# Optimization experiments

Measured on AMD Instinct MI355X. Metric: run time of the kernel, lower is better.

The kernel has to match this reference:

```python
import jax, jax.numpy as jnp
import numpy as np

NUM_EMBEDDINGS = 512
EMBEDDING_DIM = 64
COMMITMENT_COST = 0.25


def setup_inputs() -> dict:
    key = jax.random.key(0)
    k1, k2 = jax.random.split(key)
    x = jax.random.normal(k1, (32, 64, 64, 64), dtype=jnp.float32)  # [B, C=D, H, W]
    # torch init: uniform(-1/K, 1/K)
    w = jax.random.uniform(k2, (NUM_EMBEDDINGS, EMBEDDING_DIM), dtype=jnp.float32,
                           minval=-1.0 / NUM_EMBEDDINGS, maxval=1.0 / NUM_EMBEDDINGS)
    return {"x": x, "w": w}


def reference(x, w):
    # [B, C, H, W] -> [B, H, W, C]
    xt = jnp.transpose(x, (0, 2, 3, 1))
    flat = xt.reshape(-1, EMBEDDING_DIM)  # [N, D]
    # squared L2 distances to each codebook vector: [N, K]
    distances = (jnp.sum(flat * flat, axis=1, keepdims=True)
                 + jnp.sum(w * w, axis=1)
                 - 2.0 * flat @ w.T)
    idx = jnp.argmin(distances, axis=1)  # [N]
    encodings = jax.nn.one_hot(idx, NUM_EMBEDDINGS, dtype=x.dtype)  # [N, K]
    quantized = w[idx].reshape(xt.shape)  # gather == one_hot @ w
    e_latent_loss = jnp.mean((jax.lax.stop_gradient(quantized) - xt) ** 2)
    q_latent_loss = jnp.mean((quantized - jax.lax.stop_gradient(xt)) ** 2)
    quant_loss = q_latent_loss + COMMITMENT_COST * e_latent_loss
    # straight-through estimator
    quantized_st = xt + jax.lax.stop_gradient(quantized - xt)
    quantized_out = jnp.transpose(quantized_st, (0, 3, 1, 2))  # back to [B, C, H, W]
    avg_probs = jnp.mean(encodings, axis=0)
    perplexity = jnp.exp(-jnp.sum(avg_probs * jnp.log(avg_probs + 1e-10)))
    return quantized_out, quant_loss, encodings, perplexity
```

## Files before the change

### kernel.cpp

```cpp
#include <hip/hip_runtime.h>
#include <math.h>

#define TB        256
#define POSB      64
#define NPOS      131072
#define KCODES    512
#define DIM       64
#define HW        4096
#define LOSS_OFF  8388608ull
#define ENC_OFF   8388609ull
#define PERP_OFF  75497473ull
#define TILE_DW   (POSB * KCODES)
#define NF4       ((TILE_DW - 4) / 4)
#define TAU       2.0e-4f

typedef __attribute__((ext_vector_type(8))) short bf16x8;
typedef __attribute__((ext_vector_type(4))) float f32x4;

__device__ __forceinline__ float tree8(float r0, float r1, float r2, float r3,
                                       float r4, float r5, float r6, float r7) {
    return __fadd_rn(__fadd_rn(__fadd_rn(r0, r1), __fadd_rn(r2, r3)),
                     __fadd_rn(__fadd_rn(r4, r5), __fadd_rn(r6, r7)));
}

extern "C" __global__ __launch_bounds__(512)
void vq_prep(const float* __restrict__ w, float* __restrict__ ww,
             int* __restrict__ counts, float* __restrict__ lossAcc,
             unsigned short* __restrict__ wfrag)
{
    const int k = threadIdx.x;
    const float* wk = w + k * DIM;
    const int ct = k >> 4, n = k & 15;
    float r[8];
    #pragma unroll
    for (int i = 0; i < 8; ++i) {
        #pragma unroll
        for (int j = 0; j < 8; ++j) {
            const int d = i * 8 + j;
            float v = wk[d];
            float pp = __fmul_rn(v, v);
            r[j] = (i == 0) ? pp : __fadd_rn(r[j], pp);
            unsigned int hb = __float_as_uint(v) & 0xFFFF0000u;
            float rr = v - __uint_as_float(hb);
            unsigned short hs = (unsigned short)(hb >> 16);
            unsigned short ls = (unsigned short)(__float_as_uint(rr) >> 16);
            const int q = d >> 5, kk = d & 31;
            const int lf = ((kk >> 3) << 4) + n, j8 = kk & 7;
            wfrag[((((0 * 32 + ct) * 2 + q) * 64 + lf) << 3) + j8] = hs;
            wfrag[((((1 * 32 + ct) * 2 + q) * 64 + lf) << 3) + j8] = ls;
        }
    }
    ww[k] = tree8(r[0], r[1], r[2], r[3], r[4], r[5], r[6], r[7]);
    counts[k] = 0;
    if (k == 0) *lossAcc = 0.0f;
}

#define FRAG(PART, CT, Q) wf[((((PART) * 32 + (CT)) * 2 + (Q)) * 64) + l]

#define TILE6(BH0, BH1, BL0, BL1, WWK)                                        \
    acc = (f32x4){(WWK), (WWK), (WWK), (WWK)};                                \
    acc = __builtin_amdgcn_mfma_f32_16x16x32_bf16(aL0, BH0, acc, 0, 0, 0);    \
    acc = __builtin_amdgcn_mfma_f32_16x16x32_bf16(aH0, BL0, acc, 0, 0, 0);    \
    acc = __builtin_amdgcn_mfma_f32_16x16x32_bf16(aH0, BH0, acc, 0, 0, 0);    \
    acc = __builtin_amdgcn_mfma_f32_16x16x32_bf16(aL1, BH1, acc, 0, 0, 0);    \
    acc = __builtin_amdgcn_mfma_f32_16x16x32_bf16(aH1, BL1, acc, 0, 0, 0);    \
    acc = __builtin_amdgcn_mfma_f32_16x16x32_bf16(aH1, BH1, acc, 0, 0, 0);

extern "C" __global__ __launch_bounds__(TB)
__attribute__((amdgpu_waves_per_eu(3, 8)))
void vq_main(const float* __restrict__ x, const float* __restrict__ w,
             const float* __restrict__ ww, float* __restrict__ out,
             int* __restrict__ counts, float* __restrict__ lossAcc,
             const unsigned short* __restrict__ wfrag)
{
    __shared__ __align__(16) float xtile[DIM][65];
    __shared__ float wwlds[KCODES];
    __shared__ int   hcount[KCODES];
    __shared__ int   ccount[POSB];
    __shared__ int   clist[POSB * 4];
    __shared__ int   bestkL[POSB];

    const int tid = threadIdx.x;
    const int l   = tid & 63;
    const int wv  = tid >> 6;
    const int n0  = blockIdx.x * POSB;
    const int b   = n0 >> 12;
    const int hw0 = n0 & 4095;

    hcount[tid]      = 0;
    hcount[tid + TB] = 0;
    if (tid < POSB) ccount[tid] = 0;
    wwlds[tid]      = ww[tid];
    wwlds[tid + TB] = ww[tid + TB];

    const float* xb = x + ((size_t)b * DIM) * HW + hw0;
    #pragma unroll
    for (int it = 0; it < 16; ++it) {
        const int idx = it * TB + tid;
        const int d = idx >> 6, ps = idx & 63;
        xtile[d][ps] = xb[(size_t)d * HW + ps];
    }

    const size_t T0 = ENC_OFF + (size_t)blockIdx.x * TILE_DW;
    float4* zs4 = reinterpret_cast<float4*>(out + T0 + 3);
    const float4 zero4 = make_float4(0.0f, 0.0f, 0.0f, 0.0f);
    if (tid < 3)  out[T0 + tid] = 0.0f;
    if (tid == 3) out[T0 + (TILE_DW - 1)] = 0.0f;

    __syncthreads();

    bf16x8 aH0, aH1, aL0, aL1;
    {
        const int arow = wv * 16 + (l & 15);
        #pragma unroll
        for (int q = 0; q < 2; ++q) {
            #pragma unroll
            for (int j8 = 0; j8 < 8; ++j8) {
                const int d = q * 32 + ((l >> 4) << 3) + j8;
                float v = xtile[d][arow];
                float m2 = -(v + v);
                unsigned int hb = __float_as_uint(m2) & 0xFFFF0000u;
                float rr = m2 - __uint_as_float(hb);
                short hs = (short)(hb >> 16);
                short ls = (short)(__float_as_uint(rr) >> 16);
                if (q == 0) { aH0[j8] = hs; aL0[j8] = ls; }
                else        { aH1[j8] = hs; aL1[j8] = ls; }
            }
        }
    }

    const bf16x8* wf = reinterpret_cast<const bf16x8*>(wfrag);
    const int rb = wv * 16 + ((l >> 4) << 2);

    float rmin[4] = { INFINITY, INFINITY, INFINITY, INFINITY };
    {
        bf16x8 c0 = FRAG(0, 0, 0), c1 = FRAG(0, 0, 1);
        bf16x8 c2 = FRAG(1, 0, 0), c3 = FRAG(1, 0, 1);
        float wa = wwlds[(l & 15)];
        f32x4 acc;
        #pragma unroll 1
        for (int ct = 0; ct < 32; ct += 2) {
            bf16x8 n0_ = FRAG(0, ct + 1, 0), n1_ = FRAG(0, ct + 1, 1);
            bf16x8 n2_ = FRAG(1, ct + 1, 0), n3_ = FRAG(1, ct + 1, 1);
            float wb = wwlds[(ct + 1) * 16 + (l & 15)];
            TILE6(c0, c1, c2, c3, wa)
            #pragma unroll
            for (int i = 0; i < 4; ++i) rmin[i] = fminf(rmin[i], acc[i]);
            {   const int m = (ct >> 1) * TB + tid;
                if (m < NF4) zs4[m] = zero4; }
            const int t2 = (ct + 2) & 31;
            c0 = FRAG(0, t2, 0); c1 = FRAG(0, t2, 1);
            c2 = FRAG(1, t2, 0); c3 = FRAG(1, t2, 1);
            wa = wwlds[t2 * 16 + (l & 15)];
            TILE6(n0_, n1_, n2_, n3_, wb)
            #pragma unroll
            for (int i = 0; i < 4; ++i) rmin[i] = fminf(rmin[i], acc[i]);
        }
    }
    #pragma unroll
    for (int mm = 1; mm < 16; mm <<= 1) {
        #pragma unroll
        for (int i = 0; i < 4; ++i)
            rmin[i] = fminf(rmin[i], __shfl_xor(rmin[i], mm));
    }
    float thr[4];
    #pragma unroll
    for (int i = 0; i < 4; ++i) thr[i] = rmin[i] + TAU;

    {
        bf16x8 c0 = FRAG(0, 0, 0), c1 = FRAG(0, 0, 1);
        bf16x8 c2 = FRAG(1, 0, 0), c3 = FRAG(1, 0, 1);
        float wa = wwlds[(l & 15)];
        f32x4 acc;
        #pragma unroll 1
        for (int ct = 0; ct < 32; ct += 2) {
            bf16x8 n0_ = FRAG(0, ct + 1, 0), n1_ = FRAG(0, ct + 1, 1);
            bf16x8 n2_ = FRAG(1, ct + 1, 0), n3_ = FRAG(1, ct + 1, 1);
            float wb = wwlds[(ct + 1) * 16 + (l & 15)];
            TILE6(c0, c1, c2, c3, wa)
            #pragma unroll
            for (int i = 0; i < 4; ++i) {
                if (acc[i] <= thr[i]) {
                    int s = atomicAdd(&ccount[rb + i], 1);
                    if (s < 4) clist[(rb + i) * 4 + s] = ct * 16 + (l & 15);
                }
            }
            {   const int m = (16 + (ct >> 1)) * TB + tid;
                if (m < NF4) zs4[m] = zero4; }
            const int t2 = (ct + 2) & 31;
            c0 = FRAG(0, t2, 0); c1 = FRAG(0, t2, 1);
            c2 = FRAG(1, t2, 0); c3 = FRAG(1, t2, 1);
            wa = wwlds[t2 * 16 + (l & 15)];
            TILE6(n0_, n1_, n2_, n3_, wb)
            #pragma unroll
            for (int i = 0; i < 4; ++i) {
                if (acc[i] <= thr[i]) {
                    int s = atomicAdd(&ccount[rb + i], 1);
                    if (s < 4) clist[(rb + i) * 4 + s] = (ct + 1) * 16 + (l & 15);
                }
            }
        }
    }

    __syncthreads();

    if (wv == 0) {
        const int cnt = ccount[l];
        int bk;
        if (cnt == 1) {
            bk = clist[l * 4 + 0];
        } else {
            float x2c[DIM];
            float r[8];
            #pragma unroll
            for (int d = 0; d < DIM; ++d) {
                float v = xtile[d][l];
                x2c[d] = v + v;
                float pp = __fmul_rn(v, v);
                r[d & 7] = (d < 8) ? pp : __fadd_rn(r[d & 7], pp);
            }
            const float A = tree8(r[0], r[1], r[2], r[3], r[4], r[5], r[6], r[7]);
            if (cnt <= 4) {
                float bd = INFINITY; int bk2 = KCODES;
                for (int c = 0; c < cnt; ++c) {
                    const int k = clist[l * 4 + c];
                    const float* wk = w + (size_t)k * DIM;
                    float s[8];
                    #pragma unroll
                    for (int i = 0; i < 8; ++i) {
                        #pragma unroll
                        for (int j = 0; j < 8; ++j) {
                            const int d = i * 8 + j;
                            float wvv = wk[d];
                            if (i == 0) s[j] = __fmul_rn(x2c[d], wvv);
                            else        s[j] = __fmaf_rn(x2c[d], wvv, s[j]);
                        }
                    }
                    float dot  = tree8(s[0], s[1], s[2], s[3], s[4], s[5], s[6], s[7]);
                    float dist = __fadd_rn(__fadd_rn(A, wwlds[k]), -dot);
                    if (dist < bd || (dist == bd && k < bk2)) { bd = dist; bk2 = k; }
                }
                bk = bk2;
            } else {
                float bd = INFINITY; int bk2 = 0;
                #pragma unroll 1
                for (int k = 0; k < KCODES; ++k) {
                    const float* wk = w + (size_t)k * DIM;
                    float s[8];
                    #pragma unroll
                    for (int i = 0; i < 8; ++i) {
                        #pragma unroll
                        for (int j = 0; j < 8; ++j) {
                            const int d = i * 8 + j;
                            float wvv = wk[d];
                            if (i == 0) s[j] = __fmul_rn(x2c[d], wvv);
                            else        s[j] = __fmaf_rn(x2c[d], wvv, s[j]);
                        }
                    }
                    float dot  = tree8(s[0], s[1], s[2], s[3], s[4], s[5], s[6], s[7]);
                    float dist = __fadd_rn(__fadd_rn(A, wwlds[k]), -dot);
                    if (dist < bd) { bd = dist; bk2 = k; }
                }
                bk = bk2;
            }
        }
        bestkL[l] = bk;
        out[ENC_OFF + (size_t)(n0 + l) * KCODES + bk] = 1.0f;
        atomicAdd(&hcount[bk], 1);
    }

    __syncthreads();

    {
        const int sp = tid & 63, q = tid >> 6;
        const int bk = bestkL[sp];
        const float4* wr = reinterpret_cast<const float4*>(w + (size_t)bk * DIM);
        float* qo = out + ((size_t)b * DIM) * HW + (hw0 + sp);
        float sse = 0.0f;
        #pragma unroll
        for (int c = 0; c < 4; ++c) {
            float4 qv = wr[q * 4 + c];
            const int ch = q * 16 + c * 4;
            qo[(size_t)(ch + 0) * HW] = qv.x;
            qo[(size_t)(ch + 1) * HW] = qv.y;
            qo[(size_t)(ch + 2) * HW] = qv.z;
            qo[(size_t)(ch + 3) * HW] = qv.w;
            float e0 = qv.x - xtile[ch + 0][sp]; sse = __fmaf_rn(e0, e0, sse);
            float e1 = qv.y - xtile[ch + 1][sp]; sse = __fmaf_rn(e1, e1, sse);
            float e2 = qv.z - xtile[ch + 2][sp]; sse = __fmaf_rn(e2, e2, sse);
            float e3 = qv.w - xtile[ch + 3][sp]; sse = __fmaf_rn(e3, e3, sse);
        }
        #pragma unroll
        for (int off = 32; off > 0; off >>= 1) sse += __shfl_down(sse, off);
        if (l == 0) atomicAdd(lossAcc, sse);
    }

    __syncthreads();

    {
        int c0 = hcount[tid];       if (c0) atomicAdd(&counts[tid], c0);
        int c1 = hcount[tid + TB];  if (c1) atomicAdd(&counts[tid + TB], c1);
    }
}

extern "C" __global__ __launch_bounds__(512)
void vq_finalize(const int* __restrict__ counts, const float* __restrict__ lossAcc,
                 float* __restrict__ out)
{
    __shared__ double sred[KCODES];
    const int t = threadIdx.x;
    double p = (double)counts[t] * (1.0 / (double)NPOS);
    sred[t] = -p * log(p + 1e-10);
    __syncthreads();
    for (int s = KCODES / 2; s > 0; s >>= 1) {
        if (t < s) sred[t] += sred[t + s];
        __syncthreads();
    }
    if (t == 0) {
        out[PERP_OFF] = (float)exp(sred[0]);
        out[LOSS_OFF] = 1.25f * (lossAcc[0] / 8388608.0f);
    }
}

extern "C" void kernel_launch(void* const* d_in, const int* in_sizes, int n_in,
                              void* d_out, int out_size, void* d_ws, size_t ws_size,
                              hipStream_t stream)
{
    const float* x = (const float*)d_in[0];
    const float* w = (const float*)d_in[1];
    float* out = (float*)d_out;

    float* ww              = (float*)d_ws;
    int*   counts          = (int*)((char*)d_ws + 2048);
    float* lossAcc         = (float*)((char*)d_ws + 4096);
    unsigned short* wfrag  = (unsigned short*)((char*)d_ws + 8192);

    vq_prep<<<1, 512, 0, stream>>>(w, ww, counts, lossAcc, wfrag);
    vq_main<<<NPOS / POSB, TB, 0, stream>>>(x, w, ww, out, counts,
                                            lossAcc, wfrag);
    vq_finalize<<<1, 512, 0, stream>>>(counts, lossAcc, out);
}
```

Before: 439.2 us.

## Move one-hot encoding writes out of main kernel into separate streaming kernel

The main VQ kernel no longer zero-fills the 256MB one-hot encoding tile inside its MFMA loops and no longer scatters the 1.0 value. It writes each position's best code index to a small workspace buffer instead. A new kernel then writes the full encodings, each float4 computed directly from that index. This decouples the compute-bound distance search from the bandwidth-bound store, at the cost of an extra launch and a small index round-trip through global memory.

```diff
diff --git a/kernel.cpp b/kernel.cpp
--- a/kernel.cpp
+++ b/kernel.cpp
@@ -71,7 +71,8 @@
 void vq_main(const float* __restrict__ x, const float* __restrict__ w,
              const float* __restrict__ ww, float* __restrict__ out,
              int* __restrict__ counts, float* __restrict__ lossAcc,
-             const unsigned short* __restrict__ wfrag)
+             const unsigned short* __restrict__ wfrag,
+             unsigned short* __restrict__ bkg)
 {
     __shared__ __align__(16) float xtile[DIM][65];
     __shared__ float wwlds[KCODES];
@@ -100,13 +101,6 @@
         const int d = idx >> 6, ps = idx & 63;
         xtile[d][ps] = xb[(size_t)d * HW + ps];
     }
-
-    const size_t T0 = ENC_OFF + (size_t)blockIdx.x * TILE_DW;
-    float4* zs4 = reinterpret_cast<float4*>(out + T0 + 3);
-    const float4 zero4 = make_float4(0.0f, 0.0f, 0.0f, 0.0f);
-    if (tid < 3)  out[T0 + tid] = 0.0f;
-    if (tid == 3) out[T0 + (TILE_DW - 1)] = 0.0f;
-
     __syncthreads();
 
     bf16x8 aH0, aH1, aL0, aL1;
@@ -146,8 +140,6 @@
             TILE6(c0, c1, c2, c3, wa)
             #pragma unroll
             for (int i = 0; i < 4; ++i) rmin[i] = fminf(rmin[i], acc[i]);
-            {   const int m = (ct >> 1) * TB + tid;
-                if (m < NF4) zs4[m] = zero4; }
             const int t2 = (ct + 2) & 31;
             c0 = FRAG(0, t2, 0); c1 = FRAG(0, t2, 1);
             c2 = FRAG(1, t2, 0); c3 = FRAG(1, t2, 1);
@@ -185,8 +177,6 @@
                     if (s < 4) clist[(rb + i) * 4 + s] = ct * 16 + (l & 15);
                 }
             }
-            {   const int m = (16 + (ct >> 1)) * TB + tid;
-                if (m < NF4) zs4[m] = zero4; }
             const int t2 = (ct + 2) & 31;
             c0 = FRAG(0, t2, 0); c1 = FRAG(0, t2, 1);
             c2 = FRAG(1, t2, 0); c3 = FRAG(1, t2, 1);
@@ -265,7 +255,7 @@
             }
         }
         bestkL[l] = bk;
-        out[ENC_OFF + (size_t)(n0 + l) * KCODES + bk] = 1.0f;
+        bkg[n0 + l] = (unsigned short)bk;
         atomicAdd(&hcount[bk], 1);
     }
 
@@ -303,6 +293,41 @@
     }
 }
 
+extern "C" __global__ __launch_bounds__(TB)
+void vq_enc(const unsigned short* __restrict__ bkg, float* __restrict__ out)
+{
+    __shared__ int bkL[POSB];
+    const int tid = threadIdx.x;
+    const int n0  = blockIdx.x * POSB;
+    if (tid < POSB) bkL[tid] = bkg[n0 + tid];
+    const size_t T0 = ENC_OFF + (size_t)blockIdx.x * TILE_DW;
+    __syncthreads();
+
+    if (tid < 3)  out[T0 + tid] = (bkL[0] == tid) ? 1.0f : 0.0f;
+    if (tid == 3) out[T0 + (TILE_DW - 1)] = (bkL[POSB - 1] == 511) ? 1.0f : 0.0f;
+
+    float4* zs4 = reinterpret_cast<float4*>(out + T0 + 3);
+    #pragma unroll 4
+    for (int it = 0; it < 32; ++it) {
+        const int m = it * TB + tid;
+        if (m < NF4) {
+            const int o0 = 3 + 4 * m;
+            float4 v;
+            {
+                const int oa = o0,     pa = oa >> 9, ca = oa & 511;
+                const int ob = o0 + 1, pb = ob >> 9, cb = ob & 511;
+                const int oc = o0 + 2, pc = oc >> 9, cc = oc & 511;
+                const int od = o0 + 3, pd = od >> 9, cd = od & 511;
+                v.x = (bkL[pa] == ca) ? 1.0f : 0.0f;
+                v.y = (bkL[pb] == cb) ? 1.0f : 0.0f;
+                v.z = (bkL[pc] == cc) ? 1.0f : 0.0f;
+                v.w = (bkL[pd] == cd) ? 1.0f : 0.0f;
+            }
+            zs4[m] = v;
+        }
+    }
+}
+
 extern "C" __global__ __launch_bounds__(512)
 void vq_finalize(const int* __restrict__ counts, const float* __restrict__ lossAcc,
                  float* __restrict__ out)
@@ -334,9 +359,11 @@
     int*   counts          = (int*)((char*)d_ws + 2048);
     float* lossAcc         = (float*)((char*)d_ws + 4096);
     unsigned short* wfrag  = (unsigned short*)((char*)d_ws + 8192);
+    unsigned short* bkg    = (unsigned short*)((char*)d_ws + 139264);
 
     vq_prep<<<1, 512, 0, stream>>>(w, ww, counts, lossAcc, wfrag);
     vq_main<<<NPOS / POSB, TB, 0, stream>>>(x, w, ww, out, counts,
-                                            lossAcc, wfrag);
+                                            lossAcc, wfrag, bkg);
+    vq_enc<<<NPOS / POSB, TB, 0, stream>>>(bkg, out);
     vq_finalize<<<1, 512, 0, stream>>>(counts, lossAcc, out);
 }
```

New measurement: 469.2 us. 1.07x slower.

## Process 256 positions per block to reuse codebook fragments across four row tiles

Applied to the files above, without the earlier changes.

Each block now handles 256 positions instead of 64, and each wave keeps four row tiles of A fragments in registers. Every loaded codebook B fragment therefore feeds four MFMA tile groups, cutting fragment loads per position by four. The prep kernel is spread over 33 blocks and writes the bf16 hi/lo fragments as vector stores. The encoding zero-fill is reorganised for the larger tile. In exchange there is more register pressure (waves_per_eu lowered to 2), a larger LDS x tile, and four times fewer blocks, which may reduce latency hiding.

```diff
diff --git a/kernel.cpp b/kernel.cpp
--- a/kernel.cpp
+++ b/kernel.cpp
@@ -2,7 +2,7 @@
 #include <math.h>
 
 #define TB        256
-#define POSB      64
+#define POSB      256
 #define NPOS      131072
 #define KCODES    512
 #define DIM       64
@@ -28,52 +28,68 @@
              int* __restrict__ counts, float* __restrict__ lossAcc,
              unsigned short* __restrict__ wfrag)
 {
-    const int k = threadIdx.x;
-    const float* wk = w + k * DIM;
-    const int ct = k >> 4, n = k & 15;
-    float r[8];
-    #pragma unroll
-    for (int i = 0; i < 8; ++i) {
-        #pragma unroll
-        for (int j = 0; j < 8; ++j) {
-            const int d = i * 8 + j;
-            float v = wk[d];
-            float pp = __fmul_rn(v, v);
-            r[j] = (i == 0) ? pp : __fadd_rn(r[j], pp);
-            unsigned int hb = __float_as_uint(v) & 0xFFFF0000u;
-            float rr = v - __uint_as_float(hb);
-            unsigned short hs = (unsigned short)(hb >> 16);
-            unsigned short ls = (unsigned short)(__float_as_uint(rr) >> 16);
-            const int q = d >> 5, kk = d & 31;
-            const int lf = ((kk >> 3) << 4) + n, j8 = kk & 7;
-            wfrag[((((0 * 32 + ct) * 2 + q) * 64 + lf) << 3) + j8] = hs;
-            wfrag[((((1 * 32 + ct) * 2 + q) * 64 + lf) << 3) + j8] = ls;
-        }
-    }
-    ww[k] = tree8(r[0], r[1], r[2], r[3], r[4], r[5], r[6], r[7]);
-    counts[k] = 0;
-    if (k == 0) *lossAcc = 0.0f;
+    const int t = threadIdx.x;
+    if (blockIdx.x < 32) {
+        const int ct = blockIdx.x;
+        if (t < 256) {
+            const int part = t >> 7, q = (t >> 6) & 1, lf = t & 63;
+            const int n = lf & 15, k = ct * 16 + n;
+            const float* wk = w + (size_t)k * DIM;
+            unsigned short v8[8];
+            #pragma unroll
+            for (int j8 = 0; j8 < 8; ++j8) {
+                const int d = q * 32 + ((lf >> 4) << 3) + j8;
+                float v = wk[d];
+                unsigned int hb = __float_as_uint(v) & 0xFFFF0000u;
+                if (part == 0) {
+                    v8[j8] = (unsigned short)(hb >> 16);
+                } else {
+                    float rr = v - __uint_as_float(hb);
+                    v8[j8] = (unsigned short)(__float_as_uint(rr) >> 16);
+                }
+            }
+            bf16x8* dst = reinterpret_cast<bf16x8*>(wfrag);
+            dst[((part * 32 + ct) * 2 + q) * 64 + lf] =
+                *reinterpret_cast<const bf16x8*>(v8);
+        }
+    } else {
+        const int k = t;
+        const float* wk = w + (size_t)k * DIM;
+        float r[8];
+        #pragma unroll
+        for (int i = 0; i < 8; ++i) {
+            #pragma unroll
+            for (int j = 0; j < 8; ++j) {
+                float v = wk[i * 8 + j];
+                float pp = __fmul_rn(v, v);
+                r[j] = (i == 0) ? pp : __fadd_rn(r[j], pp);
+            }
+        }
+        ww[k] = tree8(r[0], r[1], r[2], r[3], r[4], r[5], r[6], r[7]);
+        counts[k] = 0;
+        if (k == 0) *lossAcc = 0.0f;
+    }
 }
 
 #define FRAG(PART, CT, Q) wf[((((PART) * 32 + (CT)) * 2 + (Q)) * 64) + l]
 
-#define TILE6(BH0, BH1, BL0, BL1, WWK)                                        \
+#define TILE6(PT, B0, B1, B2, B3, WWK)                                        \
     acc = (f32x4){(WWK), (WWK), (WWK), (WWK)};                                \
-    acc = __builtin_amdgcn_mfma_f32_16x16x32_bf16(aL0, BH0, acc, 0, 0, 0);    \
-    acc = __builtin_amdgcn_mfma_f32_16x16x32_bf16(aH0, BL0, acc, 0, 0, 0);    \
-    acc = __builtin_amdgcn_mfma_f32_16x16x32_bf16(aH0, BH0, acc, 0, 0, 0);    \
-    acc = __builtin_amdgcn_mfma_f32_16x16x32_bf16(aL1, BH1, acc, 0, 0, 0);    \
-    acc = __builtin_amdgcn_mfma_f32_16x16x32_bf16(aH1, BL1, acc, 0, 0, 0);    \
-    acc = __builtin_amdgcn_mfma_f32_16x16x32_bf16(aH1, BH1, acc, 0, 0, 0);
+    acc = __builtin_amdgcn_mfma_f32_16x16x32_bf16(aL0[PT], B0, acc, 0, 0, 0); \
+    acc = __builtin_amdgcn_mfma_f32_16x16x32_bf16(aH0[PT], B2, acc, 0, 0, 0); \
+    acc = __builtin_amdgcn_mfma_f32_16x16x32_bf16(aH0[PT], B0, acc, 0, 0, 0); \
+    acc = __builtin_amdgcn_mfma_f32_16x16x32_bf16(aL1[PT], B1, acc, 0, 0, 0); \
+    acc = __builtin_amdgcn_mfma_f32_16x16x32_bf16(aH1[PT], B3, acc, 0, 0, 0); \
+    acc = __builtin_amdgcn_mfma_f32_16x16x32_bf16(aH1[PT], B1, acc, 0, 0, 0);
 
 extern "C" __global__ __launch_bounds__(TB)
-__attribute__((amdgpu_waves_per_eu(3, 8)))
+__attribute__((amdgpu_waves_per_eu(2, 8)))
 void vq_main(const float* __restrict__ x, const float* __restrict__ w,
              const float* __restrict__ ww, float* __restrict__ out,
              int* __restrict__ counts, float* __restrict__ lossAcc,
              const unsigned short* __restrict__ wfrag)
 {
-    __shared__ __align__(16) float xtile[DIM][65];
+    __shared__ __align__(16) float xtile[DIM][POSB + 1];
     __shared__ float wwlds[KCODES];
     __shared__ int   hcount[KCODES];
     __shared__ int   ccount[POSB];
@@ -89,29 +105,23 @@
 
     hcount[tid]      = 0;
     hcount[tid + TB] = 0;
-    if (tid < POSB) ccount[tid] = 0;
-    wwlds[tid]      = ww[tid];
-    wwlds[tid + TB] = ww[tid + TB];
+    ccount[tid]      = 0;
+    wwlds[tid]       = ww[tid];
+    wwlds[tid + TB]  = ww[tid + TB];
 
     const float* xb = x + ((size_t)b * DIM) * HW + hw0;
     #pragma unroll
-    for (int it = 0; it < 16; ++it) {
+    for (int it = 0; it < 64; ++it) {
         const int idx = it * TB + tid;
-        const int d = idx >> 6, ps = idx & 63;
+        const int d = idx >> 8, ps = idx & 255;
         xtile[d][ps] = xb[(size_t)d * HW + ps];
     }
-
-    const size_t T0 = ENC_OFF + (size_t)blockIdx.x * TILE_DW;
-    float4* zs4 = reinterpret_cast<float4*>(out + T0 + 3);
-    const float4 zero4 = make_float4(0.0f, 0.0f, 0.0f, 0.0f);
-    if (tid < 3)  out[T0 + tid] = 0.0f;
-    if (tid == 3) out[T0 + (TILE_DW - 1)] = 0.0f;
-
-    __syncthreads();
-
-    bf16x8 aH0, aH1, aL0, aL1;
-    {
-        const int arow = wv * 16 + (l & 15);
+    __syncthreads();
+
+    bf16x8 aH0[4], aH1[4], aL0[4], aL1[4];
+    #pragma unroll
+    for (int pt = 0; pt < 4; ++pt) {
+        const int arow = (wv * 4 + pt) * 16 + (l & 15);
         #pragma unroll
         for (int q = 0; q < 2; ++q) {
             #pragma unroll
@@ -123,49 +133,66 @@
                 float rr = m2 - __uint_as_float(hb);
                 short hs = (short)(hb >> 16);
                 short ls = (short)(__float_as_uint(rr) >> 16);
-                if (q == 0) { aH0[j8] = hs; aL0[j8] = ls; }
-                else        { aH1[j8] = hs; aL1[j8] = ls; }
+                if (q == 0) { aH0[pt][j8] = hs; aL0[pt][j8] = ls; }
+                else        { aH1[pt][j8] = hs; aL1[pt][j8] = ls; }
             }
         }
     }
 
     const bf16x8* wf = reinterpret_cast<const bf16x8*>(wfrag);
-    const int rb = wv * 16 + ((l >> 4) << 2);
-
-    float rmin[4] = { INFINITY, INFINITY, INFINITY, INFINITY };
+    const int rloc = (l >> 4) << 2;
+
+    const size_t T0 = ENC_OFF + (size_t)blockIdx.x * TILE_DW;
+    float4* zs4 = reinterpret_cast<float4*>(out + T0 + 3);
+    const float4 zero4 = make_float4(0.0f, 0.0f, 0.0f, 0.0f);
+    if (tid < 3)  out[T0 + tid] = 0.0f;
+    if (tid == 3) out[T0 + (TILE_DW - 1)] = 0.0f;
+
+    float rmin[4][4];
+    #pragma unroll
+    for (int pt = 0; pt < 4; ++pt)
+        #pragma unroll
+        for (int i = 0; i < 4; ++i) rmin[pt][i] = INFINITY;
     {
         bf16x8 c0 = FRAG(0, 0, 0), c1 = FRAG(0, 0, 1);
         bf16x8 c2 = FRAG(1, 0, 0), c3 = FRAG(1, 0, 1);
         float wa = wwlds[(l & 15)];
         f32x4 acc;
         #pragma unroll 1
-        for (int ct = 0; ct < 32; ct += 2) {
-            bf16x8 n0_ = FRAG(0, ct + 1, 0), n1_ = FRAG(0, ct + 1, 1);
-            bf16x8 n2_ = FRAG(1, ct + 1, 0), n3_ = FRAG(1, ct + 1, 1);
-            float wb = wwlds[(ct + 1) * 16 + (l & 15)];
-            TILE6(c0, c1, c2, c3, wa)
-            #pragma unroll
-            for (int i = 0; i < 4; ++i) rmin[i] = fminf(rmin[i], acc[i]);
-            {   const int m = (ct >> 1) * TB + tid;
-                if (m < NF4) zs4[m] = zero4; }
-            const int t2 = (ct + 2) & 31;
-            c0 = FRAG(0, t2, 0); c1 = FRAG(0, t2, 1);
-            c2 = FRAG(1, t2, 0); c3 = FRAG(1, t2, 1);
-            wa = wwlds[t2 * 16 + (l & 15)];
-            TILE6(n0_, n1_, n2_, n3_, wb)
-            #pragma unroll
-            for (int i = 0; i < 4; ++i) rmin[i] = fminf(rmin[i], acc[i]);
-        }
-    }
+        for (int ct = 0; ct < 32; ++ct) {
+            const int nt = (ct + 1) & 31;
+            bf16x8 p0 = FRAG(0, nt, 0), p1 = FRAG(0, nt, 1);
+            bf16x8 p2 = FRAG(1, nt, 0), p3 = FRAG(1, nt, 1);
+            float wb = wwlds[nt * 16 + (l & 15)];
+            #pragma unroll
+            for (int pt = 0; pt < 4; ++pt) {
+                TILE6(pt, c0, c1, c2, c3, wa)
+                #pragma unroll
+                for (int i = 0; i < 4; ++i)
+                    rmin[pt][i] = fminf(rmin[pt][i], acc[i]);
+            }
+            {
+                const int mb = ct * (TB * 2) + tid;
+                zs4[mb]              = zero4;
+                zs4[mb + TB]         = zero4;
+                const int mb2 = (TB * 64) + ct * (TB * 2) + tid;
+                zs4[mb2]             = zero4;
+                zs4[mb2 + TB]        = zero4;
+            }
+            c0 = p0; c1 = p1; c2 = p2; c3 = p3; wa = wb;
+        }
+    }
+    float thr[4][4];
     #pragma unroll
-    for (int mm = 1; mm < 16; mm <<= 1) {
-        #pragma unroll
-        for (int i = 0; i < 4; ++i)
-            rmin[i] = fminf(rmin[i], __shfl_xor(rmin[i], mm));
-    }
-    float thr[4];
-    #pragma unroll
-    for (int i = 0; i < 4; ++i) thr[i] = rmin[i] + TAU;
+    for (int pt = 0; pt < 4; ++pt) {
+        #pragma unroll
+        for (int mm = 1; mm < 16; mm <<= 1)
+            #pragma unroll
+            for (int i = 0; i < 4; ++i)
+                rmin[pt][i] = fminf(rmin[pt][i], __shfl_xor(rmin[pt][i], mm));
+        #pragma unroll
+        for (int i = 0; i < 4; ++i) thr[pt][i] = rmin[pt][i] + TAU;
+    }
 
     {
         bf16x8 c0 = FRAG(0, 0, 0), c1 = FRAG(0, 0, 1);
@@ -173,48 +200,49 @@
         float wa = wwlds[(l & 15)];
         f32x4 acc;
         #pragma unroll 1
-        for (int ct = 0; ct < 32; ct += 2) {
-            bf16x8 n0_ = FRAG(0, ct + 1, 0), n1_ = FRAG(0, ct + 1, 1);
-            bf16x8 n2_ = FRAG(1, ct + 1, 0), n3_ = FRAG(1, ct + 1, 1);
-            float wb = wwlds[(ct + 1) * 16 + (l & 15)];
-            TILE6(c0, c1, c2, c3, wa)
-            #pragma unroll
-            for (int i = 0; i < 4; ++i) {
-                if (acc[i] <= thr[i]) {
-                    int s = atomicAdd(&ccount[rb + i], 1);
-                    if (s < 4) clist[(rb + i) * 4 + s] = ct * 16 + (l & 15);
+        for (int ct = 0; ct < 32; ++ct) {
+            const int nt = (ct + 1) & 31;
+            bf16x8 p0 = FRAG(0, nt, 0), p1 = FRAG(0, nt, 1);
+            bf16x8 p2 = FRAG(1, nt, 0), p3 = FRAG(1, nt, 1);
+            float wb = wwlds[nt * 16 + (l & 15)];
+            #pragma unroll
+            for (int pt = 0; pt < 4; ++pt) {
+                TILE6(pt, c0, c1, c2, c3, wa)
+                const int prow = (wv * 4 + pt) * 16 + rloc;
+                #pragma unroll
+                for (int i = 0; i < 4; ++i) {
+                    if (acc[i] <= thr[pt][i]) {
+                        int s = atomicAdd(&ccount[prow + i], 1);
+                        if (s < 4) clist[(prow + i) * 4 + s] = ct * 16 + (l & 15);
+                    }
                 }
             }
-            {   const int m = (16 + (ct >> 1)) * TB + tid;
-                if (m < NF4) zs4[m] = zero4; }
-            const int t2 = (ct + 2) & 31;
-            c0 = FRAG(0, t2, 0); c1 = FRAG(0, t2, 1);
-            c2 = FRAG(1, t2, 0); c3 = FRAG(1, t2, 1);
-            wa = wwlds[t2 * 16 + (l & 15)];
-            TILE6(n0_, n1_, n2_, n3_, wb)
-            #pragma unroll
-            for (int i = 0; i < 4; ++i) {
-                if (acc[i] <= thr[i]) {
-                    int s = atomicAdd(&ccount[rb + i], 1);
-                    if (s < 4) clist[(rb + i) * 4 + s] = (ct + 1) * 16 + (l & 15);
-                }
-            }
-        }
-    }
-
-    __syncthreads();
-
-    if (wv == 0) {
-        const int cnt = ccount[l];
+            {
+                const int mb = 16384 + ct * (TB * 2) + tid;
+                zs4[mb]       = zero4;
+                if (mb + TB < NF4) zs4[mb + TB] = zero4;
+                const int mb2 = 16384 + (TB * 64) + ct * (TB * 2) + tid;
+                if (mb2 < NF4)      zs4[mb2]      = zero4;
+                if (mb2 + TB < NF4) zs4[mb2 + TB] = zero4;
+            }
+            c0 = p0; c1 = p1; c2 = p2; c3 = p3; wa = wb;
+        }
+    }
+
+    __syncthreads();
+
+    {
+        const int p = wv * 64 + l;
+        const int cnt = ccount[p];
         int bk;
         if (cnt == 1) {
-            bk = clist[l * 4 + 0];
+            bk = clist[p * 4 + 0];
         } else {
             float x2c[DIM];
             float r[8];
             #pragma unroll
             for (int d = 0; d < DIM; ++d) {
-                float v = xtile[d][l];
+                float v = xtile[d][p];
                 x2c[d] = v + v;
                 float pp = __fmul_rn(v, v);
                 r[d & 7] = (d < 8) ? pp : __fadd_rn(r[d & 7], pp);
@@ -223,7 +251,7 @@
             if (cnt <= 4) {
                 float bd = INFINITY; int bk2 = KCODES;
                 for (int c = 0; c < cnt; ++c) {
-                    const int k = clist[l * 4 + c];
+                    const int k = clist[p * 4 + c];
                     const float* wk = w + (size_t)k * DIM;
                     float s[8];
                     #pragma unroll
@@ -264,23 +292,23 @@
                 bk = bk2;
             }
         }
-        bestkL[l] = bk;
-        out[ENC_OFF + (size_t)(n0 + l) * KCODES + bk] = 1.0f;
+        bestkL[p] = bk;
+        out[ENC_OFF + (size_t)(n0 + p) * KCODES + bk] = 1.0f;
         atomicAdd(&hcount[bk], 1);
     }
 
     __syncthreads();
 
     {
-        const int sp = tid & 63, q = tid >> 6;
+        const int sp = tid;
         const int bk = bestkL[sp];
         const float4* wr = reinterpret_cast<const float4*>(w + (size_t)bk * DIM);
         float* qo = out + ((size_t)b * DIM) * HW + (hw0 + sp);
         float sse = 0.0f;
         #pragma unroll
-        for (int c = 0; c < 4; ++c) {
-            float4 qv = wr[q * 4 + c];
-            const int ch = q * 16 + c * 4;
+        for (int c = 0; c < 16; ++c) {
+            float4 qv = wr[c];
+            const int ch = c * 4;
             qo[(size_t)(ch + 0) * HW] = qv.x;
             qo[(size_t)(ch + 1) * HW] = qv.y;
             qo[(size_t)(ch + 2) * HW] = qv.z;
@@ -335,7 +363,7 @@
     float* lossAcc         = (float*)((char*)d_ws + 4096);
     unsigned short* wfrag  = (unsigned short*)((char*)d_ws + 8192);
 
-    vq_prep<<<1, 512, 0, stream>>>(w, ww, counts, lossAcc, wfrag);
+    vq_prep<<<33, 512, 0, stream>>>(w, ww, counts, lossAcc, wfrag);
     vq_main<<<NPOS / POSB, TB, 0, stream>>>(x, w, ww, out, counts,
                                             lossAcc, wfrag);
     vq_finalize<<<1, 512, 0, stream>>>(counts, lossAcc, out);
```

After: 392.4 us. 1.12x faster.
